# Kernel optimization log

Hardware: AMD Instinct MI355X
Metric: run time of the kernel (lower is better)

Reference implementation:

```python
import jax, jax.numpy as jnp
import numpy as np

B, F0, D = 2048, 40, 32
LAYER0, LAYER1 = 128, 128  # layer_size=(128,128), split_half=True -> field_nums=[40,64]


def setup_inputs() -> dict:
    key = jax.random.key(0)
    k1, k2, k3 = jax.random.split(key, 3)
    x = jax.random.normal(k1, (B, F0, D), dtype=jnp.float32)
    # TF conv1d filters: [1, F_prev*F0, size]; we store them reshaped [F0, F_prev_fields, size]
    # Layer 0: F_prev = F0 = 40 -> W0 flattened index m = i*F0 + j, i over x0 fields, j over hidden fields
    W0 = jax.random.normal(k2, (F0, F0, LAYER0), dtype=jnp.float32) * 0.05
    b0 = jnp.zeros((LAYER0,), dtype=jnp.float32)
    # Layer 1: F_prev = LAYER0 // 2 = 64 (split_half)
    W1 = jax.random.normal(k3, (F0, LAYER0 // 2, LAYER1), dtype=jnp.float32) * 0.05
    b1 = jnp.zeros((LAYER1,), dtype=jnp.float32)
    return {"x": x, "W0": W0, "b0": b0, "W1": W1, "b1": b1}


def reference(x, W0, b0, W1, b1):
    # CIN layer 0: outer product x0 (x) x0 over fields per embedding dim, then 1x1 conv + bias + relu
    # TF flattens dot_result as index i*F_prev + j, matching W0[i, j, s].
    h0 = jax.nn.relu(jnp.einsum('bid,bjd,ijs->bsd', x, x, W0) + b0[None, :, None])  # (B, 128, D)
    half = LAYER0 // 2
    next_hidden, direct0 = h0[:, :half, :], h0[:, half:, :]  # split_half
    # CIN layer 1 (last layer): all feature maps go to direct connect
    direct1 = jax.nn.relu(
        jnp.einsum('bid,bjd,ijs->bsd', x, next_hidden, W1) + b1[None, :, None]
    )  # (B, 128, D)
    result = jnp.concatenate([direct0, direct1], axis=1)  # (B, 192, D)
    return jnp.sum(result, axis=-1)  # (B, 192)
```

## Files before the change

### kernel.cpp

```cpp
#include <hip/hip_runtime.h>
#include <stdint.h>


typedef __attribute__((ext_vector_type(8))) short short8;
typedef __attribute__((ext_vector_type(4))) float f32x4;

__device__ __forceinline__ float bf2f(unsigned short v) {
    return __uint_as_float(((unsigned int)v) << 16);
}
__device__ __forceinline__ unsigned short f2bf(float f) {
    unsigned int u = __float_as_uint(f);
    u += 0x7FFFu + ((u >> 16) & 1u);
    return (unsigned short)(u >> 16);
}
__device__ __forceinline__ unsigned int packhu(float lo, float hi) {
    unsigned int a = __float_as_uint(lo) + 0x8000u;
    unsigned int b = __float_as_uint(hi) + 0x8000u;
    return __builtin_amdgcn_perm(b, a, 0x07060302u);
}
__device__ __forceinline__ float qsum(float v) {
    v += __shfl_xor(v, 16, 64);
    v += __shfl_xor(v, 32, 64);
    return v;
}

__global__ void permute_w_both(const float* __restrict__ W0, const float* __restrict__ W1,
                               unsigned short* __restrict__ Wp0, unsigned short* __restrict__ Wp1)
{
    int e = blockIdx.x;
    int s = threadIdx.x;
    if (e < 1600) {
        int i = e / 40, j = e - i * 40;
        int t = (j >> 3) * 10 + (i >> 2);
        int kl = (i & 3) * 8 + (j & 7);
        Wp0[t * 4096 + s * 32 + kl] = f2bf(W0[(size_t)e * 128 + s]);
    } else {
        int e1 = e - 1600;
        int i = e1 >> 6, j = e1 & 63;
        int t = (j >> 3) * 10 + (i >> 2);
        int kl = (i & 3) * 8 + (j & 7);
        Wp1[t * 4096 + s * 32 + kl] = f2bf(W1[(size_t)e1 * 128 + s]);
    }
}

template<int NJC>
__device__ __forceinline__ void gemm_phase_reg(
    const unsigned short* __restrict__ Wp,
    const unsigned short* __restrict__ Jl,
    int jstride,
    const float xi[4][10],
    f32x4 acc[4][4], int tid)
{
    const int lane = tid & 63;
    const int mw = (tid >> 6) & 1;
    const int nw = tid >> 7;
    const int ml = lane & 15;
    const int kc = lane >> 4;
    const unsigned short* wt = Wp + ((nw * 64 + ml) * 32 + kc * 8);
    const unsigned short* jrow[4];
    #pragma unroll
    for (int mt = 0; mt < 4; ++mt)
        jrow[mt] = Jl + (mw * 64 + mt * 16 + ml) * jstride;

    uint4 bv[4];
    #pragma unroll
    for (int nt = 0; nt < 4; ++nt) bv[nt] = *(const uint4*)(wt + nt * 512);

    for (int jc = 0; jc < NJC; ++jc) {
        float xj[4][8];
        #pragma unroll
        for (int mt = 0; mt < 4; ++mt) {
            uint4 jv = *(const uint4*)(jrow[mt] + jc * 8);
            xj[mt][0] = __uint_as_float(jv.x << 16);
            xj[mt][1] = __uint_as_float(jv.x & 0xFFFF0000u);
            xj[mt][2] = __uint_as_float(jv.y << 16);
            xj[mt][3] = __uint_as_float(jv.y & 0xFFFF0000u);
            xj[mt][4] = __uint_as_float(jv.z << 16);
            xj[mt][5] = __uint_as_float(jv.z & 0xFFFF0000u);
            xj[mt][6] = __uint_as_float(jv.w << 16);
            xj[mt][7] = __uint_as_float(jv.w & 0xFFFF0000u);
        }
        #pragma unroll
        for (int ic = 0; ic < 10; ++ic) {
            const unsigned short* wn;
            if (ic < 9) wn = wt + 4096;
            else        wn = (jc + 1 < NJC) ? wt + 4096 : wt;
            uint4 bn[4];
            #pragma unroll
            for (int nt = 0; nt < 4; ++nt) bn[nt] = *(const uint4*)(wn + nt * 512);
            uint4 av[4];
            #pragma unroll
            for (int mt = 0; mt < 4; ++mt) {
                float xs = xi[mt][ic];
                av[mt].x = packhu(xs * xj[mt][0], xs * xj[mt][1]);
                av[mt].y = packhu(xs * xj[mt][2], xs * xj[mt][3]);
                av[mt].z = packhu(xs * xj[mt][4], xs * xj[mt][5]);
                av[mt].w = packhu(xs * xj[mt][6], xs * xj[mt][7]);
            }
            #pragma unroll
            for (int mt = 0; mt < 4; ++mt)
                #pragma unroll
                for (int nt = 0; nt < 4; ++nt)
                    acc[mt][nt] = __builtin_amdgcn_mfma_f32_16x16x32_bf16(
                        __builtin_bit_cast(short8, av[mt]),
                        __builtin_bit_cast(short8, bv[nt]),
                        acc[mt][nt], 0, 0, 0);
            #pragma unroll
            for (int nt = 0; nt < 4; ++nt) bv[nt] = bn[nt];
            wt = wn;
        }
    }
}

__global__ __launch_bounds__(256, 2)
void fused_two_layer(const float* __restrict__ x,
                     const unsigned short* __restrict__ W0p,
                     const float* __restrict__ b0,
                     const unsigned short* __restrict__ W1p,
                     const float* __restrict__ b1,
                     float* __restrict__ out)
{
    __shared__ __align__(16) unsigned short Xl[128 * 40];
    __shared__ __align__(16) unsigned short NH[128 * 72];

    const int tid  = threadIdx.x;
    const int lane = tid & 63;
    const int mw   = (tid >> 6) & 1;
    const int nw   = tid >> 7;
    const int ml   = lane & 15;
    const int kc   = lane >> 4;

    const float* xblk = x + (size_t)blockIdx.x * (4 * 40 * 32);
    #pragma unroll
    for (int bl = 0; bl < 4; ++bl) {
        #pragma unroll
        for (int k = 0; k < 5; ++k) {
            int e = 256 * k + tid;
            int i = e >> 5, d = e & 31;
            Xl[(bl * 32 + d) * 40 + i] = f2bf(xblk[bl * 1280 + e]);
        }
    }
    __syncthreads();

    float xi[4][10];
    #pragma unroll
    for (int mt = 0; mt < 4; ++mt) {
        const unsigned short* xr = Xl + (mw * 64 + mt * 16 + ml) * 40;
        #pragma unroll
        for (int ic = 0; ic < 10; ++ic) xi[mt][ic] = bf2f(xr[ic * 4 + kc]);
    }

    f32x4 acc[4][4];
    const f32x4 zero4 = {0.f, 0.f, 0.f, 0.f};
    #pragma unroll
    for (int mt = 0; mt < 4; ++mt)
        #pragma unroll
        for (int nt = 0; nt < 4; ++nt) acc[mt][nt] = zero4;

    gemm_phase_reg<5>(W0p, Xl, 40, xi, acc, tid);

    {
        float bias[4];
        #pragma unroll
        for (int nt = 0; nt < 4; ++nt) bias[nt] = b0[nw * 64 + nt * 16 + ml];
        if (nw == 0) {
            #pragma unroll
            for (int mt = 0; mt < 4; ++mt) {
                int r = mw * 64 + mt * 16 + (kc << 2);
                #pragma unroll
                for (int nt = 0; nt < 4; ++nt) {
                    int s = nt * 16 + ml;
                    #pragma unroll
                    for (int rg = 0; rg < 4; ++rg) {
                        float v = fmaxf(acc[mt][nt][rg] + bias[nt], 0.0f);
                        NH[(r + rg) * 72 + s] = f2bf(v);
                    }
                }
            }
        } else {
            int bb = blockIdx.x * 4 + mw * 2;
            #pragma unroll
            for (int nt = 0; nt < 4; ++nt) {
                float sA = 0.f, sB = 0.f;
                #pragma unroll
                for (int rg = 0; rg < 4; ++rg) {
                    sA += fmaxf(acc[0][nt][rg] + bias[nt], 0.f) + fmaxf(acc[1][nt][rg] + bias[nt], 0.f);
                    sB += fmaxf(acc[2][nt][rg] + bias[nt], 0.f) + fmaxf(acc[3][nt][rg] + bias[nt], 0.f);
                }
                sA = qsum(sA); sB = qsum(sB);
                if (lane < 16) {
                    out[(size_t)bb * 192 + nt * 16 + lane]       = sA;
                    out[(size_t)(bb + 1) * 192 + nt * 16 + lane] = sB;
                }
            }
        }
    }
    __syncthreads();

    #pragma unroll
    for (int mt = 0; mt < 4; ++mt)
        #pragma unroll
        for (int nt = 0; nt < 4; ++nt) acc[mt][nt] = zero4;

    gemm_phase_reg<8>(W1p, NH, 72, xi, acc, tid);

    {
        float bias[4];
        #pragma unroll
        for (int nt = 0; nt < 4; ++nt) bias[nt] = b1[nw * 64 + nt * 16 + ml];
        int bb = blockIdx.x * 4 + mw * 2;
        #pragma unroll
        for (int nt = 0; nt < 4; ++nt) {
            float sA = 0.f, sB = 0.f;
            #pragma unroll
            for (int rg = 0; rg < 4; ++rg) {
                sA += fmaxf(acc[0][nt][rg] + bias[nt], 0.f) + fmaxf(acc[1][nt][rg] + bias[nt], 0.f);
                sB += fmaxf(acc[2][nt][rg] + bias[nt], 0.f) + fmaxf(acc[3][nt][rg] + bias[nt], 0.f);
            }
            sA = qsum(sA); sB = qsum(sB);
            if (lane < 16) {
                out[(size_t)bb * 192 + 64 + nw * 64 + nt * 16 + lane]       = sA;
                out[(size_t)(bb + 1) * 192 + 64 + nw * 64 + nt * 16 + lane] = sB;
            }
        }
    }
}

extern "C" void kernel_launch(void* const* d_in, const int* in_sizes, int n_in,
                              void* d_out, int out_size, void* d_ws, size_t ws_size,
                              hipStream_t stream) {
    const float* x  = (const float*)d_in[0];
    const float* W0 = (const float*)d_in[1];
    const float* b0 = (const float*)d_in[2];
    const float* W1 = (const float*)d_in[3];
    const float* b1 = (const float*)d_in[4];
    float* out = (float*)d_out;

    unsigned short* W0p = (unsigned short*)d_ws;
    unsigned short* W1p = (unsigned short*)((char*)d_ws + 50 * 4096 * 2);

    permute_w_both<<<1600 + 2560, 128, 0, stream>>>(W0, W1, W0p, W1p);
    fused_two_layer<<<512, 256, 0, stream>>>(x, W0p, b0, W1p, b1, out);
}
```

Baseline: 138.0 us.

## Switch operands to fp16 with packed half2 products, vectorize weight permute

Measured after the change: 129.0 us. 6.6% less time.

```diff
diff --git a/kernel.cpp b/kernel.cpp
--- a/kernel.cpp
+++ b/kernel.cpp
@@ -2,21 +2,12 @@
 #include <stdint.h>
 
 
-typedef __attribute__((ext_vector_type(8))) short short8;
+typedef __attribute__((ext_vector_type(8))) _Float16 half8;
+typedef __attribute__((ext_vector_type(2))) _Float16 half2v;
 typedef __attribute__((ext_vector_type(4))) float f32x4;
 
-__device__ __forceinline__ float bf2f(unsigned short v) {
-    return __uint_as_float(((unsigned int)v) << 16);
-}
-__device__ __forceinline__ unsigned short f2bf(float f) {
-    unsigned int u = __float_as_uint(f);
-    u += 0x7FFFu + ((u >> 16) & 1u);
-    return (unsigned short)(u >> 16);
-}
-__device__ __forceinline__ unsigned int packhu(float lo, float hi) {
-    unsigned int a = __float_as_uint(lo) + 0x8000u;
-    unsigned int b = __float_as_uint(hi) + 0x8000u;
-    return __builtin_amdgcn_perm(b, a, 0x07060302u);
+__device__ __forceinline__ unsigned short f2h(float f) {
+    return __builtin_bit_cast(unsigned short, (_Float16)f);
 }
 __device__ __forceinline__ float qsum(float v) {
     v += __shfl_xor(v, 16, 64);
@@ -27,20 +18,22 @@
 __global__ void permute_w_both(const float* __restrict__ W0, const float* __restrict__ W1,
                                unsigned short* __restrict__ Wp0, unsigned short* __restrict__ Wp1)
 {
-    int e = blockIdx.x;
-    int s = threadIdx.x;
-    if (e < 1600) {
-        int i = e / 40, j = e - i * 40;
-        int t = (j >> 3) * 10 + (i >> 2);
-        int kl = (i & 3) * 8 + (j & 7);
-        Wp0[t * 4096 + s * 32 + kl] = f2bf(W0[(size_t)e * 128 + s]);
-    } else {
-        int e1 = e - 1600;
-        int i = e1 >> 6, j = e1 & 63;
-        int t = (j >> 3) * 10 + (i >> 2);
-        int kl = (i & 3) * 8 + (j & 7);
-        Wp1[t * 4096 + s * 32 + kl] = f2bf(W1[(size_t)e1 * 128 + s]);
-    }
+    int t = blockIdx.x;
+    int s = threadIdx.x >> 1, h = threadIdx.x & 1;
+    const float* W; unsigned short* Wp; int JW, tt;
+    if (t < 50) { W = W0; Wp = Wp0; JW = 40; tt = t; }
+    else        { W = W1; Wp = Wp1; JW = 64; tt = t - 50; }
+    int jc = tt / 10, ic = tt - jc * 10;
+    unsigned short outv[16];
+    #pragma unroll
+    for (int q = 0; q < 16; ++q) {
+        int kl = h * 16 + q;
+        int i = ic * 4 + (kl >> 3), j = jc * 8 + (kl & 7);
+        outv[q] = f2h(W[((size_t)(i * JW + j)) * 128 + s]);
+    }
+    unsigned short* dst = Wp + (size_t)tt * 4096 + s * 32 + h * 16;
+    *(uint4*)dst       = *(const uint4*)outv;
+    *(uint4*)(dst + 8) = *(const uint4*)(outv + 8);
 }
 
 template<int NJC>
@@ -48,7 +41,7 @@
     const unsigned short* __restrict__ Wp,
     const unsigned short* __restrict__ Jl,
     int jstride,
-    const float xi[4][10],
+    const unsigned int xi2[4][10],
     f32x4 acc[4][4], int tid)
 {
     const int lane = tid & 63;
@@ -66,19 +59,17 @@
     #pragma unroll
     for (int nt = 0; nt < 4; ++nt) bv[nt] = *(const uint4*)(wt + nt * 512);
 
+    uint4 jv[4], jvn[4];
+    #pragma unroll
+    for (int mt = 0; mt < 4; ++mt) jv[mt] = *(const uint4*)(jrow[mt]);
+
     for (int jc = 0; jc < NJC; ++jc) {
-        float xj[4][8];
-        #pragma unroll
-        for (int mt = 0; mt < 4; ++mt) {
-            uint4 jv = *(const uint4*)(jrow[mt] + jc * 8);
-            xj[mt][0] = __uint_as_float(jv.x << 16);
-            xj[mt][1] = __uint_as_float(jv.x & 0xFFFF0000u);
-            xj[mt][2] = __uint_as_float(jv.y << 16);
-            xj[mt][3] = __uint_as_float(jv.y & 0xFFFF0000u);
-            xj[mt][4] = __uint_as_float(jv.z << 16);
-            xj[mt][5] = __uint_as_float(jv.z & 0xFFFF0000u);
-            xj[mt][6] = __uint_as_float(jv.w << 16);
-            xj[mt][7] = __uint_as_float(jv.w & 0xFFFF0000u);
+        if (jc + 1 < NJC) {
+            #pragma unroll
+            for (int mt = 0; mt < 4; ++mt) jvn[mt] = *(const uint4*)(jrow[mt] + (jc + 1) * 8);
+        } else {
+            #pragma unroll
+            for (int mt = 0; mt < 4; ++mt) jvn[mt] = jv[mt];
         }
         #pragma unroll
         for (int ic = 0; ic < 10; ++ic) {
@@ -91,24 +82,30 @@
             uint4 av[4];
             #pragma unroll
             for (int mt = 0; mt < 4; ++mt) {
-                float xs = xi[mt][ic];
-                av[mt].x = packhu(xs * xj[mt][0], xs * xj[mt][1]);
-                av[mt].y = packhu(xs * xj[mt][2], xs * xj[mt][3]);
-                av[mt].z = packhu(xs * xj[mt][4], xs * xj[mt][5]);
-                av[mt].w = packhu(xs * xj[mt][6], xs * xj[mt][7]);
+                half2v x2 = __builtin_bit_cast(half2v, xi2[mt][ic]);
+                av[mt].x = __builtin_bit_cast(unsigned int,
+                    (half2v)(x2 * __builtin_bit_cast(half2v, jv[mt].x)));
+                av[mt].y = __builtin_bit_cast(unsigned int,
+                    (half2v)(x2 * __builtin_bit_cast(half2v, jv[mt].y)));
+                av[mt].z = __builtin_bit_cast(unsigned int,
+                    (half2v)(x2 * __builtin_bit_cast(half2v, jv[mt].z)));
+                av[mt].w = __builtin_bit_cast(unsigned int,
+                    (half2v)(x2 * __builtin_bit_cast(half2v, jv[mt].w)));
             }
             #pragma unroll
             for (int mt = 0; mt < 4; ++mt)
                 #pragma unroll
                 for (int nt = 0; nt < 4; ++nt)
-                    acc[mt][nt] = __builtin_amdgcn_mfma_f32_16x16x32_bf16(
-                        __builtin_bit_cast(short8, av[mt]),
-                        __builtin_bit_cast(short8, bv[nt]),
+                    acc[mt][nt] = __builtin_amdgcn_mfma_f32_16x16x32_f16(
+                        __builtin_bit_cast(half8, av[mt]),
+                        __builtin_bit_cast(half8, bv[nt]),
                         acc[mt][nt], 0, 0, 0);
             #pragma unroll
             for (int nt = 0; nt < 4; ++nt) bv[nt] = bn[nt];
             wt = wn;
         }
+        #pragma unroll
+        for (int mt = 0; mt < 4; ++mt) jv[mt] = jvn[mt];
     }
 }
 
@@ -137,17 +134,20 @@
         for (int k = 0; k < 5; ++k) {
             int e = 256 * k + tid;
             int i = e >> 5, d = e & 31;
-            Xl[(bl * 32 + d) * 40 + i] = f2bf(xblk[bl * 1280 + e]);
+            Xl[(bl * 32 + d) * 40 + i] = f2h(xblk[bl * 1280 + e]);
         }
     }
     __syncthreads();
 
-    float xi[4][10];
+    unsigned int xi2[4][10];
     #pragma unroll
     for (int mt = 0; mt < 4; ++mt) {
         const unsigned short* xr = Xl + (mw * 64 + mt * 16 + ml) * 40;
         #pragma unroll
-        for (int ic = 0; ic < 10; ++ic) xi[mt][ic] = bf2f(xr[ic * 4 + kc]);
+        for (int ic = 0; ic < 10; ++ic) {
+            unsigned int u = xr[ic * 4 + kc];
+            xi2[mt][ic] = u | (u << 16);
+        }
     }
 
     f32x4 acc[4][4];
@@ -157,7 +157,7 @@
         #pragma unroll
         for (int nt = 0; nt < 4; ++nt) acc[mt][nt] = zero4;
 
-    gemm_phase_reg<5>(W0p, Xl, 40, xi, acc, tid);
+    gemm_phase_reg<5>(W0p, Xl, 40, xi2, acc, tid);
 
     {
         float bias[4];
@@ -173,7 +173,7 @@
                     #pragma unroll
                     for (int rg = 0; rg < 4; ++rg) {
                         float v = fmaxf(acc[mt][nt][rg] + bias[nt], 0.0f);
-                        NH[(r + rg) * 72 + s] = f2bf(v);
+                        NH[(r + rg) * 72 + s] = f2h(v);
                     }
                 }
             }
@@ -202,7 +202,7 @@
         #pragma unroll
         for (int nt = 0; nt < 4; ++nt) acc[mt][nt] = zero4;
 
-    gemm_phase_reg<8>(W1p, NH, 72, xi, acc, tid);
+    gemm_phase_reg<8>(W1p, NH, 72, xi2, acc, tid);
 
     {
         float bias[4];
@@ -239,6 +239,6 @@
     unsigned short* W0p = (unsigned short*)d_ws;
     unsigned short* W1p = (unsigned short*)((char*)d_ws + 50 * 4096 * 2);
 
-    permute_w_both<<<1600 + 2560, 128, 0, stream>>>(W0, W1, W0p, W1p);
+    permute_w_both<<<130, 256, 0, stream>>>(W0, W1, W0p, W1p);
     fused_two_layer<<<512, 256, 0, stream>>>(x, W0p, b0, W1p, b1, out);
 }
```
